# Kernel tuning notes

Measured on AMD Instinct MI355X. Metric: run time of the kernel, lower is better.

Reference implementation:

```python
import jax, jax.numpy as jnp
import numpy as np

B, T, I, H, L, O = 64, 512, 64, 512, 3, 1


def setup_inputs() -> dict:
    key = jax.random.key(0)
    ks = jax.random.split(key, 4 * L + 3)
    inp = {"x": jax.random.normal(ks[0], (B, T, I), dtype=jnp.float32)}
    s = 1.0 / np.sqrt(H)  # PyTorch LSTM init scale
    kidx = 1
    for l in range(L):
        in_dim = I if l == 0 else H
        inp[f"W_ih{l}"] = jax.random.uniform(ks[kidx], (4 * H, in_dim), minval=-s, maxval=s); kidx += 1
        inp[f"W_hh{l}"] = jax.random.uniform(ks[kidx], (4 * H, H), minval=-s, maxval=s); kidx += 1
        inp[f"b_ih{l}"] = jax.random.uniform(ks[kidx], (4 * H,), minval=-s, maxval=s); kidx += 1
        inp[f"b_hh{l}"] = jax.random.uniform(ks[kidx], (4 * H,), minval=-s, maxval=s); kidx += 1
    inp["fc_w"] = jax.random.uniform(ks[kidx], (O, H), minval=-s, maxval=s)
    inp["fc_b"] = jax.random.uniform(ks[kidx + 1], (O,), minval=-s, maxval=s)
    return inp


def _lstm_layer(x, W_ih, W_hh, b_ih, b_hh):
    # x: [B, T, in_dim] -> hidden trajectory [B, T, H]
    b, _, _ = x.shape
    h_dim = W_hh.shape[1]
    # precompute all input-to-hidden projections in one big GEMM
    xg = jnp.einsum('bti,gi->btg', x, W_ih) + b_ih + b_hh  # [B, T, 4H]

    def step(carry, xg_t):
        h, c = carry
        gates = xg_t + h @ W_hh.T  # [B, 4H]
        i, f, g, o = jnp.split(gates, 4, axis=-1)  # PyTorch gate order i,f,g,o
        i = jax.nn.sigmoid(i)
        f = jax.nn.sigmoid(f)
        g = jnp.tanh(g)
        o = jax.nn.sigmoid(o)
        c = f * c + i * g
        h = o * jnp.tanh(c)
        return (h, c), h

    init = (jnp.zeros((b, h_dim), x.dtype), jnp.zeros((b, h_dim), x.dtype))
    _, hs = jax.lax.scan(step, init, jnp.swapaxes(xg, 0, 1))  # time-major scan
    return jnp.swapaxes(hs, 0, 1)  # back to [B, T, H]


def reference(x, W_ih0, W_hh0, b_ih0, b_hh0, W_ih1, W_hh1, b_ih1, b_hh1,
              W_ih2, W_hh2, b_ih2, b_hh2, fc_w, fc_b):
    # 3-layer LSTM (eval mode: inter-layer dropout=0.2 is identity) + fc on last step
    h = _lstm_layer(x, W_ih0, W_hh0, b_ih0, b_hh0)
    h = _lstm_layer(h, W_ih1, W_hh1, b_ih1, b_hh1)
    h = _lstm_layer(h, W_ih2, W_hh2, b_ih2, b_hh2)
    return h[:, -1, :] @ fc_w.T + fc_b  # [B, O]
```

## Files before the change

kernel.cpp:

```cpp
#include <hip/hip_runtime.h>
#include <math.h>

#define BB 64
#define TT 512
#define II 64
#define HH 512
#define NBLK 192
#define FLAG_STRIDE 32

typedef __attribute__((ext_vector_type(8))) _Float16 f16x8;
typedef __attribute__((ext_vector_type(16))) float f32x16;

__device__ __forceinline__ float sigmoidf_(float x) {
    return 1.0f / (1.0f + expf(-x));
}

__device__ __forceinline__ void store8_thru(void* p, unsigned long long u) {
    __hip_atomic_store((unsigned long long*)p, u, __ATOMIC_RELAXED, __HIP_MEMORY_SCOPE_AGENT);
}
__device__ __forceinline__ void storef_thru(float* p, float v) {
    __hip_atomic_store(p, v, __ATOMIC_RELAXED, __HIP_MEMORY_SCOPE_AGENT);
}
__device__ __forceinline__ float loadf_byp(const float* p) {
    return __hip_atomic_load(p, __ATOMIC_RELAXED, __HIP_MEMORY_SCOPE_AGENT);
}
__device__ __forceinline__ void storeu_thru(unsigned* p, unsigned v) {
    __hip_atomic_store(p, v, __ATOMIC_RELAXED, __HIP_MEMORY_SCOPE_AGENT);
}
__device__ __forceinline__ unsigned loadu_byp(const unsigned* p) {
    return __hip_atomic_load(p, __ATOMIC_RELAXED, __HIP_MEMORY_SCOPE_AGENT);
}

__device__ __forceinline__ void poll_ge64(const unsigned* flags, unsigned tgt) {
    const int lane = threadIdx.x & 63;
    const unsigned* a = flags + (size_t)lane * FLAG_STRIDE;
    unsigned f = loadu_byp(a);
    while (__ballot(f < tgt) != 0ull) {
        __builtin_amdgcn_s_sleep(1);
        f = loadu_byp(a);
    }
}

struct B8 { f16x8 v0, v1, v2, v3, v4, v5, v6, v7; };

__device__ __forceinline__ void issue8(const char* rb, B8& b) {
    const char* p0 = rb;
    const char* p1 = rb + 2048;
    const char* p2 = rb + 4096;
    const char* p3 = rb + 6144;
    const char* p4 = rb + 8192;
    const char* p5 = rb + 10240;
    const char* p6 = rb + 12288;
    const char* p7 = rb + 14336;
    asm volatile(
        "global_load_dwordx4 %0, %8, off sc0 sc1\n\t"
        "global_load_dwordx4 %1, %9, off sc0 sc1\n\t"
        "global_load_dwordx4 %2, %10, off sc0 sc1\n\t"
        "global_load_dwordx4 %3, %11, off sc0 sc1\n\t"
        "global_load_dwordx4 %4, %12, off sc0 sc1\n\t"
        "global_load_dwordx4 %5, %13, off sc0 sc1\n\t"
        "global_load_dwordx4 %6, %14, off sc0 sc1\n\t"
        "global_load_dwordx4 %7, %15, off sc0 sc1"
        : "=&v"(b.v0), "=&v"(b.v1), "=&v"(b.v2), "=&v"(b.v3),
          "=&v"(b.v4), "=&v"(b.v5), "=&v"(b.v6), "=&v"(b.v7)
        : "v"(p0), "v"(p1), "v"(p2), "v"(p3), "v"(p4), "v"(p5), "v"(p6), "v"(p7));
}

#define DEF_WAIT(NAME, CNT) \
__device__ __forceinline__ void NAME(B8& b) { \
    asm volatile("s_waitcnt vmcnt(" #CNT ")" \
        : "+v"(b.v0), "+v"(b.v1), "+v"(b.v2), "+v"(b.v3), \
          "+v"(b.v4), "+v"(b.v5), "+v"(b.v6), "+v"(b.v7)); \
    __builtin_amdgcn_sched_barrier(0); \
}
DEF_WAIT(wait16, 16)
DEF_WAIT(wait8, 8)
DEF_WAIT(wait0, 0)

#define MFMA_F16 __builtin_amdgcn_mfma_f32_32x32x16_f16

template<int S0>
__device__ __forceinline__ void consume8(const char* wa_h, const char* wa_l, const B8& b,
                                         f32x16& c0, f32x16& c2) {
#define KSTEP(J, BV) { \
    f16x8 ahi = *(const f16x8*)(wa_h + (size_t)(S0 + J) * 2048); \
    f16x8 alo = *(const f16x8*)(wa_l + (size_t)(S0 + J) * 2048); \
    c0 = MFMA_F16(ahi, BV, c0, 0, 0, 0); \
    c2 = MFMA_F16(alo, BV, c2, 0, 0, 0); }
    KSTEP(0, b.v0) KSTEP(1, b.v1) KSTEP(2, b.v2) KSTEP(3, b.v3)
    KSTEP(4, b.v4) KSTEP(5, b.v5) KSTEP(6, b.v6) KSTEP(7, b.v7)
#undef KSTEP
}

template<int S0>
__device__ __forceinline__ void panel32(const char* rb,
                                        const char* wa_h, const char* wa_l,
                                        f32x16& c0, f32x16& c2) {
    B8 A, B, C;
    issue8(rb, A);
    issue8(rb + 16384, B);
    issue8(rb + 32768, C);
    wait16(A); consume8<S0>(wa_h, wa_l, A, c0, c2);
    issue8(rb + 49152, A);
    wait16(B); consume8<S0 + 8>(wa_h, wa_l, B, c0, c2);
    wait8(C);  consume8<S0 + 16>(wa_h, wa_l, C, c0, c2);
    wait0(A);  consume8<S0 + 24>(wa_h, wa_l, A, c0, c2);
}
template<int S0>
__device__ __forceinline__ void panel16(const char* rb,
                                        const char* wa_h, const char* wa_l,
                                        f32x16& c0, f32x16& c2) {
    B8 A, B;
    issue8(rb, A);
    issue8(rb + 16384, B);
    wait8(A); consume8<S0>(wa_h, wa_l, A, c0, c2);
    wait0(B); consume8<S0 + 8>(wa_h, wa_l, B, c0, c2);
}

__global__ __launch_bounds__(256) void pack_x(const float* __restrict__ x,
                                              char* __restrict__ xTq) {
    const int t = blockIdx.x;
    const int b = threadIdx.x & 63;
    const int gq = threadIdx.x >> 6;
    #pragma unroll
    for (int gi = 0; gi < 2; ++gi) {
        const int g2 = gq + gi * 4;
        const float* src = x + ((size_t)b * TT + t) * II + g2 * 8;
        float w[8];
        *(float4*)&w[0] = *(const float4*)src;
        *(float4*)&w[4] = *(const float4*)(src + 4);
        f16x8 hv;
        #pragma unroll
        for (int j = 0; j < 8; ++j) hv[j] = (_Float16)w[j];
        *(f16x8*)(xTq + (((size_t)t * 8 + g2) * 64 + b) * 16) = hv;
    }
}

template<int IN_DIM, int NKS>
__device__ void pack_weights(const float* __restrict__ Wih, const float* __restrict__ Whh,
                             int hbase, char* __restrict__ WAc) {
    const int lane = threadIdx.x & 63;
    const int wq = threadIdx.x >> 6;
    const int m = lane & 31;
    const int lg = lane >> 5;
    const int swz = (lane & 28) << 2;
    const int off_h = (lane * 32) ^ swz;
    const int off_l = (lane * 32 + 16) ^ swz;
    const int grow = (m >> 3) * HH + hbase + (m & 7);
    const float* wi = Wih + (size_t)grow * IN_DIM;
    const float* wh = Whh + (size_t)grow * HH;
    for (int s = wq; s < NKS; s += 4) {
        const int k8 = s * 16 + lg * 8;
        const float* src = (k8 < IN_DIM) ? (wi + k8) : (wh + (k8 - IN_DIM));
        float w[8];
        *(float4*)&w[0] = *(const float4*)src;
        *(float4*)&w[4] = *(const float4*)(src + 4);
        f16x8 hv, lv;
        #pragma unroll
        for (int j = 0; j < 8; ++j) {
            _Float16 h = (_Float16)w[j];
            hv[j] = h;
            lv[j] = (_Float16)(w[j] - (float)h);
        }
        char* dst = WAc + (size_t)s * 2048;
        *(f16x8*)(dst + off_h) = hv;
        *(f16x8*)(dst + off_l) = lv;
    }
}

template<int LAYER, int IN_DIM, int NKS, int KH>
__device__ void lstm_core(int tile,
                          const char* __restrict__ xTq,
                          const char* __restrict__ hbuf_prev, char* __restrict__ hbuf,
                          float* __restrict__ h2last, unsigned* __restrict__ flags,
                          const float* __restrict__ Wih, const float* __restrict__ Whh,
                          const float* __restrict__ bih, const float* __restrict__ bhh,
                          char* __restrict__ WAc, float* __restrict__ redbuf) {
    const int tid = threadIdx.x;
    const int lane = tid & 63;
    const int wq = tid >> 6;
    const int ntile = wq & 1;
    const int khalf = wq >> 1;
    const int lg = lane >> 5;
    const int b = ntile * 32 + (lane & 31);
    const int hbase = tile * 8;

    pack_weights<IN_DIM, NKS>(Wih, Whh, hbase, WAc);

    float bias_v[16];
    float cst[4] = {0.f, 0.f, 0.f, 0.f};
    if (khalf == 0) {
        #pragma unroll
        for (int g = 0; g < 4; ++g)
            #pragma unroll
            for (int j = 0; j < 4; ++j) {
                const int grow = g * HH + hbase + j + 4 * lg;
                bias_v[g * 4 + j] = bih[grow] + bhh[grow];
            }
    }
    __syncthreads();

    const int swz = (lane & 28) << 2;
    const char* wa_h = WAc + ((lane * 32) ^ swz);
    const char* wa_l = WAc + ((lane * 32 + 16) ^ swz);

    unsigned* const arr_own  = flags + (size_t)(LAYER * 64) * FLAG_STRIDE;
    const unsigned* arr_prev = (LAYER > 0) ? flags + (size_t)((LAYER - 1) * 64) * FLAG_STRIDE : arr_own;
    const unsigned* arr_next = (LAYER < 2) ? flags + (size_t)((LAYER + 1) * 64) * FLAG_STRIDE : arr_own;
    unsigned* const my_flag  = arr_own + (size_t)tile * FLAG_STRIDE;
    const int xoff = lg * 1024 + b * 16;

    for (int t = 0; t < TT; ++t) {
        f32x16 c0 = {0,0,0,0,0,0,0,0,0,0,0,0,0,0,0,0};
        f32x16 c2 = c0;
        const char* rb_h = hbuf + (size_t)(t & 1) * 65536 + xoff;
        const char* rb_x = hbuf_prev + (size_t)((t + 1) & 1) * 65536 + xoff;

        if (khalf == 0) {
            if (LAYER == 0) {
                const char* xq = xTq + (size_t)t * 8192 + xoff;
                #pragma unroll
                for (int s = 0; s < 4; ++s) {
                    f16x8 bv = *(const f16x8*)(xq + (size_t)s * 2048);
                    f16x8 ahi = *(const f16x8*)(wa_h + (size_t)s * 2048);
                    f16x8 alo = *(const f16x8*)(wa_l + (size_t)s * 2048);
                    c0 = MFMA_F16(ahi, bv, c0, 0, 0, 0);
                    c2 = MFMA_F16(alo, bv, c2, 0, 0, 0);
                }
                if (t > 0) {
                    poll_ge64(arr_own, (unsigned)t);
                    panel16<4>(rb_h, wa_h, wa_l, c0, c2);
                }
            } else {
                poll_ge64(arr_prev, (unsigned)(t + 1));
                panel32<0>(rb_x, wa_h, wa_l, c0, c2);
            }
        } else {
            if (t > 0) {
                poll_ge64(arr_own, (unsigned)t);
                if (LAYER == 0) panel16<20>(rb_h + 32768, wa_h, wa_l, c0, c2);
                else            panel32<32>(rb_h, wa_h, wa_l, c0, c2);
            }
        }

        f32x16 cs = c0 + c2;

        if (khalf == 1) {
            float* pw = &redbuf[((size_t)ntile * 64 + lane) * 20];
            #pragma unroll
            for (int q = 0; q < 4; ++q) {
                float4 v; v.x = cs[q*4+0]; v.y = cs[q*4+1]; v.z = cs[q*4+2]; v.w = cs[q*4+3];
                *(float4*)(pw + q * 4) = v;
            }
        }
        __syncthreads();
        if (khalf == 0) {
            const float* pr = &redbuf[((size_t)ntile * 64 + lane) * 20];
            float prv[16];
            #pragma unroll
            for (int q = 0; q < 4; ++q)
                *(float4*)&prv[q * 4] = *(const float4*)(pr + q * 4);
            float gate[16];
            #pragma unroll
            for (int r = 0; r < 16; ++r) gate[r] = cs[r] + prv[r] + bias_v[r];

            union { _Float16 h[4]; unsigned long long u; } hp;
            #pragma unroll
            for (int j = 0; j < 4; ++j) {
                const float iv = sigmoidf_(gate[0 + j]);
                const float fv = sigmoidf_(gate[4 + j]);
                const float gv = tanhf(gate[8 + j]);
                const float ov = sigmoidf_(gate[12 + j]);
                cst[j] = fv * cst[j] + iv * gv;
                const float hv = ov * tanhf(cst[j]);
                hp.h[j] = (_Float16)hv;
                if (LAYER == 2 && t == TT - 1)
                    storef_thru(h2last + (size_t)(hbase + j + 4 * lg) * 64 + b, hv);
            }

            if (LAYER < 2 && t >= 2) poll_ge64(arr_next, (unsigned)(t - 1));
            char* d2 = hbuf + (size_t)((t + 1) & 1) * 65536 + (size_t)tile * 1024 + b * 16 + lg * 8;
            store8_thru(d2, hp.u);
        }
        __builtin_amdgcn_s_waitcnt(0);
        __syncthreads();
        if (tid == 0) storeu_thru(my_flag, (unsigned)(t + 1));
    }
}

__global__ __launch_bounds__(256, 1) void lstm_wavefront(
    const char* __restrict__ xTq,
    char* __restrict__ hbuf0, char* __restrict__ hbuf1, char* __restrict__ hbuf2,
    float* __restrict__ h2last, unsigned* __restrict__ flags,
    const float* __restrict__ Wih0, const float* __restrict__ Whh0,
    const float* __restrict__ bih0, const float* __restrict__ bhh0,
    const float* __restrict__ Wih1, const float* __restrict__ Whh1,
    const float* __restrict__ bih1, const float* __restrict__ bhh1,
    const float* __restrict__ Wih2, const float* __restrict__ Whh2,
    const float* __restrict__ bih2, const float* __restrict__ bhh2,
    const float* __restrict__ fcw, const float* __restrict__ fcb,
    float* __restrict__ out) {

    __shared__ short WA[64 * 64 * 16];
    __shared__ float redbuf[2 * 64 * 20];
    __shared__ float fcred[256];

    const int l = blockIdx.x >> 6;
    const int tile = blockIdx.x & 63;
    char* WAc = (char*)WA;

    if (l == 0)
        lstm_core<0, II, 36, 20>(tile, xTq, nullptr, hbuf0, h2last, flags,
                                 Wih0, Whh0, bih0, bhh0, WAc, redbuf);
    else if (l == 1)
        lstm_core<1, HH, 64, 32>(tile, xTq, hbuf0, hbuf1, h2last, flags,
                                 Wih1, Whh1, bih1, bhh1, WAc, redbuf);
    else
        lstm_core<2, HH, 64, 32>(tile, xTq, hbuf1, hbuf2, h2last, flags,
                                 Wih2, Whh2, bih2, bhh2, WAc, redbuf);

    if (blockIdx.x == 0) {
        if (threadIdx.x < 64)
            poll_ge64(flags + (size_t)(2 * 64) * FLAG_STRIDE, (unsigned)TT);
        __syncthreads();
        const int tid = threadIdx.x;
        const int b = tid & 63, kq = tid >> 6;
        float s = 0.f;
        const float* hp = h2last + (size_t)kq * 128 * 64 + b;
        const float* wp = fcw + kq * 128;
        #pragma unroll 8
        for (int k = 0; k < 128; ++k)
            s = fmaf(loadf_byp(hp + (size_t)k * 64), wp[k], s);
        fcred[tid] = s;
        __syncthreads();
        if (tid < 64)
            out[tid] = fcred[tid] + fcred[64 + tid] + fcred[128 + tid] + fcred[192 + tid] + fcb[0];
    }
}

extern "C" void kernel_launch(void* const* d_in, const int* in_sizes, int n_in,
                              void* d_out, int out_size, void* d_ws, size_t ws_size,
                              hipStream_t stream) {
    (void)in_sizes; (void)n_in; (void)out_size; (void)ws_size;

    const float* x    = (const float*)d_in[0];
    const float* Wih0 = (const float*)d_in[1];
    const float* Whh0 = (const float*)d_in[2];
    const float* bih0 = (const float*)d_in[3];
    const float* bhh0 = (const float*)d_in[4];
    const float* Wih1 = (const float*)d_in[5];
    const float* Whh1 = (const float*)d_in[6];
    const float* bih1 = (const float*)d_in[7];
    const float* bhh1 = (const float*)d_in[8];
    const float* Wih2 = (const float*)d_in[9];
    const float* Whh2 = (const float*)d_in[10];
    const float* bih2 = (const float*)d_in[11];
    const float* bhh2 = (const float*)d_in[12];
    const float* fcw  = (const float*)d_in[13];
    const float* fcb  = (const float*)d_in[14];

    char* ws = (char*)d_ws;
    unsigned* flags = (unsigned*)ws;
    char* hbuf0   = ws + 65536;
    char* hbuf1   = hbuf0 + 2 * 64 * 64 * 16;
    char* hbuf2   = hbuf1 + 2 * 64 * 64 * 16;
    float* h2last = (float*)(hbuf2 + 2 * 64 * 64 * 16);
    char* xTq     = (char*)h2last + 512 * 64 * 4;

    hipMemsetAsync(ws, 0, 65536, stream);

    pack_x<<<TT, 256, 0, stream>>>(x, xTq);

    lstm_wavefront<<<NBLK, 256, 0, stream>>>(
        xTq, hbuf0, hbuf1, hbuf2, h2last, flags,
        Wih0, Whh0, bih0, bhh0,
        Wih1, Whh1, bih1, bhh1,
        Wih2, Whh2, bih2, bhh2,
        fcw, fcb, (float*)d_out);
}
```

Before: 2.615 ms.

## Drop split-fp16 weight compensation and give each block sixteen hidden units

Weights were stored as an fp16 hi/lo pair to approximate fp32 accuracy. They are now stored as a single fp16 value. The freed LDS and MFMA slots hold a second 8-unit hidden tile, so each block covers 16 hidden units and each layer needs only 32 blocks instead of 64. Flag polling, the reduction buffer, bias and cell state all grow to cover two tiles. This cuts the number of blocks taking part in the per-timestep cross-block synchronisation, at the cost of lower weight precision in the recurrent and input GEMMs.

```diff
diff --git a/kernel.cpp b/kernel.cpp
--- a/kernel.cpp
+++ b/kernel.cpp
@@ -5,7 +5,8 @@
 #define TT 512
 #define II 64
 #define HH 512
-#define NBLK 192
+#define NBPL 32
+#define NBLK 96
 #define FLAG_STRIDE 32
 
 typedef __attribute__((ext_vector_type(8))) _Float16 f16x8;
@@ -31,8 +32,8 @@
     return __hip_atomic_load(p, __ATOMIC_RELAXED, __HIP_MEMORY_SCOPE_AGENT);
 }
 
-__device__ __forceinline__ void poll_ge64(const unsigned* flags, unsigned tgt) {
-    const int lane = threadIdx.x & 63;
+__device__ __forceinline__ void poll_ge32(const unsigned* flags, unsigned tgt) {
+    const int lane = threadIdx.x & 31;
     const unsigned* a = flags + (size_t)lane * FLAG_STRIDE;
     unsigned f = loadu_byp(a);
     while (__ballot(f < tgt) != 0ull) {
@@ -80,41 +81,39 @@
 #define MFMA_F16 __builtin_amdgcn_mfma_f32_32x32x16_f16
 
 template<int S0>
-__device__ __forceinline__ void consume8(const char* wa_h, const char* wa_l, const B8& b,
-                                         f32x16& c0, f32x16& c2) {
+__device__ __forceinline__ void consume8(const char* wa, const B8& b,
+                                         f32x16& c0, f32x16& c1) {
 #define KSTEP(J, BV) { \
-    f16x8 ahi = *(const f16x8*)(wa_h + (size_t)(S0 + J) * 2048); \
-    f16x8 alo = *(const f16x8*)(wa_l + (size_t)(S0 + J) * 2048); \
-    c0 = MFMA_F16(ahi, BV, c0, 0, 0, 0); \
-    c2 = MFMA_F16(alo, BV, c2, 0, 0, 0); }
+    f16x8 a0 = *(const f16x8*)(wa + (size_t)(S0 + J) * 2048); \
+    f16x8 a1 = *(const f16x8*)(wa + (size_t)(S0 + J) * 2048 + 1024); \
+    c0 = MFMA_F16(a0, BV, c0, 0, 0, 0); \
+    c1 = MFMA_F16(a1, BV, c1, 0, 0, 0); }
     KSTEP(0, b.v0) KSTEP(1, b.v1) KSTEP(2, b.v2) KSTEP(3, b.v3)
     KSTEP(4, b.v4) KSTEP(5, b.v5) KSTEP(6, b.v6) KSTEP(7, b.v7)
 #undef KSTEP
 }
 
 template<int S0>
-__device__ __forceinline__ void panel32(const char* rb,
-                                        const char* wa_h, const char* wa_l,
-                                        f32x16& c0, f32x16& c2) {
+__device__ __forceinline__ void panel32(const char* rb, const char* wa,
+                                        f32x16& c0, f32x16& c1) {
     B8 A, B, C;
     issue8(rb, A);
     issue8(rb + 16384, B);
     issue8(rb + 32768, C);
-    wait16(A); consume8<S0>(wa_h, wa_l, A, c0, c2);
+    wait16(A); consume8<S0>(wa, A, c0, c1);
     issue8(rb + 49152, A);
-    wait16(B); consume8<S0 + 8>(wa_h, wa_l, B, c0, c2);
-    wait8(C);  consume8<S0 + 16>(wa_h, wa_l, C, c0, c2);
-    wait0(A);  consume8<S0 + 24>(wa_h, wa_l, A, c0, c2);
+    wait16(B); consume8<S0 + 8>(wa, B, c0, c1);
+    wait8(C);  consume8<S0 + 16>(wa, C, c0, c1);
+    wait0(A);  consume8<S0 + 24>(wa, A, c0, c1);
 }
 template<int S0>
-__device__ __forceinline__ void panel16(const char* rb,
-                                        const char* wa_h, const char* wa_l,
-                                        f32x16& c0, f32x16& c2) {
+__device__ __forceinline__ void panel16(const char* rb, const char* wa,
+                                        f32x16& c0, f32x16& c1) {
     B8 A, B;
     issue8(rb, A);
     issue8(rb + 16384, B);
-    wait8(A); consume8<S0>(wa_h, wa_l, A, c0, c2);
-    wait0(B); consume8<S0 + 8>(wa_h, wa_l, B, c0, c2);
+    wait8(A); consume8<S0>(wa, A, c0, c1);
+    wait0(B); consume8<S0 + 8>(wa, B, c0, c1);
 }
 
 __global__ __launch_bounds__(256) void pack_x(const float* __restrict__ x,
@@ -138,33 +137,25 @@
 
 template<int IN_DIM, int NKS>
 __device__ void pack_weights(const float* __restrict__ Wih, const float* __restrict__ Whh,
-                             int hbase, char* __restrict__ WAc) {
+                             int hbase16, char* __restrict__ WAc) {
     const int lane = threadIdx.x & 63;
     const int wq = threadIdx.x >> 6;
-    const int m = lane & 31;
-    const int lg = lane >> 5;
-    const int swz = (lane & 28) << 2;
-    const int off_h = (lane * 32) ^ swz;
-    const int off_l = (lane * 32 + 16) ^ swz;
-    const int grow = (m >> 3) * HH + hbase + (m & 7);
-    const float* wi = Wih + (size_t)grow * IN_DIM;
-    const float* wh = Whh + (size_t)grow * HH;
-    for (int s = wq; s < NKS; s += 4) {
-        const int k8 = s * 16 + lg * 8;
-        const float* src = (k8 < IN_DIM) ? (wi + k8) : (wh + (k8 - IN_DIM));
+    const int r = lane & 31;
+    for (int sm = wq; sm < 2 * NKS; sm += 4) {
+        const int s = sm >> 1;
+        const int m = sm & 1;
+        const int grow = (r >> 3) * HH + hbase16 + m * 8 + (r & 7);
+        const int k8 = s * 16 + (lane >> 5) * 8;
+        const float* src = (k8 < IN_DIM)
+            ? (Wih + (size_t)grow * IN_DIM + k8)
+            : (Whh + (size_t)grow * HH + (k8 - IN_DIM));
         float w[8];
         *(float4*)&w[0] = *(const float4*)src;
         *(float4*)&w[4] = *(const float4*)(src + 4);
-        f16x8 hv, lv;
+        f16x8 hv;
         #pragma unroll
-        for (int j = 0; j < 8; ++j) {
-            _Float16 h = (_Float16)w[j];
-            hv[j] = h;
-            lv[j] = (_Float16)(w[j] - (float)h);
-        }
-        char* dst = WAc + (size_t)s * 2048;
-        *(f16x8*)(dst + off_h) = hv;
-        *(f16x8*)(dst + off_l) = lv;
+        for (int j = 0; j < 8; ++j) hv[j] = (_Float16)w[j];
+        *(f16x8*)(WAc + (size_t)s * 2048 + m * 1024 + lane * 16) = hv;
     }
 }
 
@@ -183,36 +174,34 @@
     const int khalf = wq >> 1;
     const int lg = lane >> 5;
     const int b = ntile * 32 + (lane & 31);
-    const int hbase = tile * 8;
-
-    pack_weights<IN_DIM, NKS>(Wih, Whh, hbase, WAc);
-
-    float bias_v[16];
-    float cst[4] = {0.f, 0.f, 0.f, 0.f};
+    const int hbase16 = tile * 16;
+
+    pack_weights<IN_DIM, NKS>(Wih, Whh, hbase16, WAc);
+
+    float bias_v[32];
+    float cst[8] = {0.f, 0.f, 0.f, 0.f, 0.f, 0.f, 0.f, 0.f};
     if (khalf == 0) {
         #pragma unroll
-        for (int g = 0; g < 4; ++g)
-            #pragma unroll
-            for (int j = 0; j < 4; ++j) {
-                const int grow = g * HH + hbase + j + 4 * lg;
-                bias_v[g * 4 + j] = bih[grow] + bhh[grow];
+        for (int m = 0; m < 2; ++m)
+            #pragma unroll
+            for (int r = 0; r < 16; ++r) {
+                const int grow = (r >> 2) * HH + hbase16 + m * 8 + (r & 3) + 4 * lg;
+                bias_v[m * 16 + r] = bih[grow] + bhh[grow];
             }
     }
     __syncthreads();
 
-    const int swz = (lane & 28) << 2;
-    const char* wa_h = WAc + ((lane * 32) ^ swz);
-    const char* wa_l = WAc + ((lane * 32 + 16) ^ swz);
-
-    unsigned* const arr_own  = flags + (size_t)(LAYER * 64) * FLAG_STRIDE;
-    const unsigned* arr_prev = (LAYER > 0) ? flags + (size_t)((LAYER - 1) * 64) * FLAG_STRIDE : arr_own;
-    const unsigned* arr_next = (LAYER < 2) ? flags + (size_t)((LAYER + 1) * 64) * FLAG_STRIDE : arr_own;
+    const char* wa = WAc + lane * 16;
+
+    unsigned* const arr_own  = flags + (size_t)(LAYER * NBPL) * FLAG_STRIDE;
+    const unsigned* arr_prev = (LAYER > 0) ? flags + (size_t)((LAYER - 1) * NBPL) * FLAG_STRIDE : arr_own;
+    const unsigned* arr_next = (LAYER < 2) ? flags + (size_t)((LAYER + 1) * NBPL) * FLAG_STRIDE : arr_own;
     unsigned* const my_flag  = arr_own + (size_t)tile * FLAG_STRIDE;
     const int xoff = lg * 1024 + b * 16;
 
     for (int t = 0; t < TT; ++t) {
         f32x16 c0 = {0,0,0,0,0,0,0,0,0,0,0,0,0,0,0,0};
-        f32x16 c2 = c0;
+        f32x16 c1 = c0;
         const char* rb_h = hbuf + (size_t)(t & 1) * 65536 + xoff;
         const char* rb_x = hbuf_prev + (size_t)((t + 1) & 1) * 65536 + xoff;
 
@@ -222,65 +211,70 @@
                 #pragma unroll
                 for (int s = 0; s < 4; ++s) {
                     f16x8 bv = *(const f16x8*)(xq + (size_t)s * 2048);
-                    f16x8 ahi = *(const f16x8*)(wa_h + (size_t)s * 2048);
-                    f16x8 alo = *(const f16x8*)(wa_l + (size_t)s * 2048);
-                    c0 = MFMA_F16(ahi, bv, c0, 0, 0, 0);
-                    c2 = MFMA_F16(alo, bv, c2, 0, 0, 0);
+                    f16x8 a0 = *(const f16x8*)(wa + (size_t)s * 2048);
+                    f16x8 a1 = *(const f16x8*)(wa + (size_t)s * 2048 + 1024);
+                    c0 = MFMA_F16(a0, bv, c0, 0, 0, 0);
+                    c1 = MFMA_F16(a1, bv, c1, 0, 0, 0);
                 }
                 if (t > 0) {
-                    poll_ge64(arr_own, (unsigned)t);
-                    panel16<4>(rb_h, wa_h, wa_l, c0, c2);
+                    poll_ge32(arr_own, (unsigned)t);
+                    panel16<4>(rb_h, wa, c0, c1);
                 }
             } else {
-                poll_ge64(arr_prev, (unsigned)(t + 1));
-                panel32<0>(rb_x, wa_h, wa_l, c0, c2);
+                poll_ge32(arr_prev, (unsigned)(t + 1));
+                panel32<0>(rb_x, wa, c0, c1);
             }
         } else {
             if (t > 0) {
-                poll_ge64(arr_own, (unsigned)t);
-                if (LAYER == 0) panel16<20>(rb_h + 32768, wa_h, wa_l, c0, c2);
-                else            panel32<32>(rb_h, wa_h, wa_l, c0, c2);
+                poll_ge32(arr_own, (unsigned)t);
+                if (LAYER == 0) panel16<20>(rb_h + 32768, wa, c0, c1);
+                else            panel32<32>(rb_h, wa, c0, c1);
             }
         }
 
-        f32x16 cs = c0 + c2;
-
         if (khalf == 1) {
-            float* pw = &redbuf[((size_t)ntile * 64 + lane) * 20];
+            float* pw = &redbuf[((size_t)ntile * 64 + lane) * 36];
             #pragma unroll
             for (int q = 0; q < 4; ++q) {
-                float4 v; v.x = cs[q*4+0]; v.y = cs[q*4+1]; v.z = cs[q*4+2]; v.w = cs[q*4+3];
+                float4 v; v.x = c0[q*4+0]; v.y = c0[q*4+1]; v.z = c0[q*4+2]; v.w = c0[q*4+3];
                 *(float4*)(pw + q * 4) = v;
+            }
+            #pragma unroll
+            for (int q = 0; q < 4; ++q) {
+                float4 v; v.x = c1[q*4+0]; v.y = c1[q*4+1]; v.z = c1[q*4+2]; v.w = c1[q*4+3];
+                *(float4*)(pw + 16 + q * 4) = v;
             }
         }
         __syncthreads();
         if (khalf == 0) {
-            const float* pr = &redbuf[((size_t)ntile * 64 + lane) * 20];
-            float prv[16];
-            #pragma unroll
-            for (int q = 0; q < 4; ++q)
+            const float* pr = &redbuf[((size_t)ntile * 64 + lane) * 36];
+            float prv[32];
+            #pragma unroll
+            for (int q = 0; q < 8; ++q)
                 *(float4*)&prv[q * 4] = *(const float4*)(pr + q * 4);
-            float gate[16];
-            #pragma unroll
-            for (int r = 0; r < 16; ++r) gate[r] = cs[r] + prv[r] + bias_v[r];
-
-            union { _Float16 h[4]; unsigned long long u; } hp;
-            #pragma unroll
-            for (int j = 0; j < 4; ++j) {
-                const float iv = sigmoidf_(gate[0 + j]);
-                const float fv = sigmoidf_(gate[4 + j]);
-                const float gv = tanhf(gate[8 + j]);
-                const float ov = sigmoidf_(gate[12 + j]);
-                cst[j] = fv * cst[j] + iv * gv;
-                const float hv = ov * tanhf(cst[j]);
-                hp.h[j] = (_Float16)hv;
-                if (LAYER == 2 && t == TT - 1)
-                    storef_thru(h2last + (size_t)(hbase + j + 4 * lg) * 64 + b, hv);
-            }
-
-            if (LAYER < 2 && t >= 2) poll_ge64(arr_next, (unsigned)(t - 1));
-            char* d2 = hbuf + (size_t)((t + 1) & 1) * 65536 + (size_t)tile * 1024 + b * 16 + lg * 8;
-            store8_thru(d2, hp.u);
+
+            if (LAYER < 2 && t >= 2) poll_ge32(arr_next, (unsigned)(t - 1));
+
+            #pragma unroll
+            for (int m = 0; m < 2; ++m) {
+                const f32x16& cs = (m == 0) ? c0 : c1;
+                union { _Float16 h[4]; unsigned long long u; } hp;
+                #pragma unroll
+                for (int j = 0; j < 4; ++j) {
+                    const float iv = sigmoidf_(cs[0 + j]  + prv[m*16 + 0 + j]  + bias_v[m*16 + 0 + j]);
+                    const float fv = sigmoidf_(cs[4 + j]  + prv[m*16 + 4 + j]  + bias_v[m*16 + 4 + j]);
+                    const float gv = tanhf   (cs[8 + j]  + prv[m*16 + 8 + j]  + bias_v[m*16 + 8 + j]);
+                    const float ov = sigmoidf_(cs[12 + j] + prv[m*16 + 12 + j] + bias_v[m*16 + 12 + j]);
+                    cst[m*4 + j] = fv * cst[m*4 + j] + iv * gv;
+                    const float hv = ov * tanhf(cst[m*4 + j]);
+                    hp.h[j] = (_Float16)hv;
+                    if (LAYER == 2 && t == TT - 1)
+                        storef_thru(h2last + (size_t)(hbase16 + m*8 + j + 4*lg) * 64 + b, hv);
+                }
+                char* d2 = hbuf + (size_t)((t + 1) & 1) * 65536
+                         + (size_t)(tile * 2 + m) * 1024 + b * 16 + lg * 8;
+                store8_thru(d2, hp.u);
+            }
         }
         __builtin_amdgcn_s_waitcnt(0);
         __syncthreads();
@@ -301,13 +295,12 @@
     const float* __restrict__ fcw, const float* __restrict__ fcb,
     float* __restrict__ out) {
 
-    __shared__ short WA[64 * 64 * 16];
-    __shared__ float redbuf[2 * 64 * 20];
+    __shared__ char WAc[64 * 2048];
+    __shared__ float redbuf[2 * 64 * 36];
     __shared__ float fcred[256];
 
-    const int l = blockIdx.x >> 6;
-    const int tile = blockIdx.x & 63;
-    char* WAc = (char*)WA;
+    const int l = blockIdx.x >> 5;
+    const int tile = blockIdx.x & 31;
 
     if (l == 0)
         lstm_core<0, II, 36, 20>(tile, xTq, nullptr, hbuf0, h2last, flags,
@@ -321,7 +314,7 @@
 
     if (blockIdx.x == 0) {
         if (threadIdx.x < 64)
-            poll_ge64(flags + (size_t)(2 * 64) * FLAG_STRIDE, (unsigned)TT);
+            poll_ge32(flags + (size_t)(2 * NBPL) * FLAG_STRIDE, (unsigned)TT);
         __syncthreads();
         const int tid = threadIdx.x;
         const int b = tid & 63, kq = tid >> 6;
@@ -367,7 +360,8 @@
     float* h2last = (float*)(hbuf2 + 2 * 64 * 64 * 16);
     char* xTq     = (char*)h2last + 512 * 64 * 4;
 
-    hipMemsetAsync(ws, 0, 65536, stream);
+    hipError_t err = hipMemsetAsync(ws, 0, 65536, stream);
+    (void)err;
 
     pack_x<<<TT, 256, 0, stream>>>(x, xTq);
 
```

Measured after the change: 3.100 ms. 1.19x slower.
